# Optimization experiments

Measured on AMD Instinct MI355X. Metric: run time of the kernel, lower is better.

Reference implementation:

```python
import jax, jax.numpy as jnp
import numpy as np

BB_SCALE_TYPE = 'MinMax'  # init kwarg; one of MinMax/Min/Max


def _unproject_all(depth_map, intrinsics):
    # depth_map: [H, W]; returns per-pixel 3D points [H, W, 3]
    H, W = depth_map.shape
    fx, fy, cx, cy = intrinsics[0], intrinsics[1], intrinsics[2], intrinsics[3]
    xs = jnp.arange(W, dtype=depth_map.dtype)[None, :]   # x_d (column)
    ys = jnp.arange(H, dtype=depth_map.dtype)[:, None]   # y_d (row)
    x3 = (xs - cx) * depth_map / fx
    y3 = (ys - cy) * depth_map / fy
    return jnp.stack([x3, y3, depth_map], axis=-1)  # [H, W, 3]


def _scale_to_unit(points, mask):
    # points: [H, W, 3]; mask: [H, W] bool. Masked bbox min/max then norm.
    m = mask[..., None]
    big = jnp.asarray(jnp.finfo(points.dtype).max, points.dtype)
    max_b = jnp.max(jnp.where(m, points, -big), axis=(0, 1))  # [3]
    min_b = jnp.min(jnp.where(m, points, big), axis=(0, 1))   # [3]
    if BB_SCALE_TYPE == 'MinMax':
        return jnp.linalg.norm(max_b - min_b)
    if BB_SCALE_TYPE == 'Min':
        return jnp.linalg.norm(min_b)
    return jnp.linalg.norm(max_b)


def setup_inputs() -> dict:
    key = jax.random.key(0)
    k1, k2, k3 = jax.random.split(key, 3)
    H, W = 2048, 2048
    depth_estimations = jax.random.uniform(k1, (1, 1, H, W), jnp.float32) * 10.0 + 0.1
    sparse_depths = jax.random.uniform(k2, (1, 1, H, W), jnp.float32) * 10.0 + 0.1
    sparse_depth_masks = jax.random.randint(k3, (1, 1, H, W), 0, 2, jnp.int32)
    intrinsics = jnp.array([500.0, 500.0, 1024.0, 1024.0], jnp.float32)  # fx, fy, cx, cy
    return {
        'depth_estimations': depth_estimations,
        'sparse_depths': sparse_depths,
        'sparse_depth_masks': sparse_depth_masks,
        'intrinsics': intrinsics,
    }


def reference(depth_estimations, sparse_depths, sparse_depth_masks, intrinsics):
    mask = sparse_depth_masks[0, 0] != 0  # [H, W]
    pts_sparse = _unproject_all(sparse_depths[0, 0], intrinsics)
    pts_dense = _unproject_all(depth_estimations[0, 0], intrinsics)
    scale_sparse = _scale_to_unit(pts_sparse, mask)
    scale_dense = _scale_to_unit(pts_dense, mask)
    rescaled_depth = (scale_sparse / scale_dense) * depth_estimations
    std = jnp.asarray(1.0, depth_estimations.dtype)
    return (rescaled_depth, std)
```

## Files before the change

### kernel.cpp

```cpp
#include <hip/hip_runtime.h>
#include <float.h>
#include <math.h>

static constexpr int H    = 2048;
static constexpr int Wd   = 2048;
static constexpr int NPIX = H * Wd;
static constexpr int BT   = 256;
static constexpr int N4   = NPIX / 4;

static constexpr int NB1   = 1024;
static constexpr int ITER1 = N4 / (NB1 * BT);

static constexpr int NB2   = 2048;
static constexpr int ITER2 = N4 / (NB2 * BT);


__global__ __launch_bounds__(BT) void reduce_bbox_kernel(
    const float* __restrict__ dense,
    const float* __restrict__ sparse,
    const int*   __restrict__ mask,
    const float* __restrict__ intr,
    float* __restrict__ ws)
{
    const float cx = intr[2], cy = intr[3];
    const float qnan = __uint_as_float(0x7FC00000u);

    float loc[12];
#pragma unroll
    for (int s = 0; s < 12; ++s) loc[s] = ((s % 6) < 3) ? FLT_MAX : -FLT_MAX;

    const float4* d4 = (const float4*)dense;
    const float4* s4 = (const float4*)sparse;
    const int4*   m4 = (const int4*)mask;

    const int tid = blockIdx.x * BT + threadIdx.x;

#pragma unroll
    for (int k = 0; k < ITER1; ++k) {
        const int i = tid + k * (NB1 * BT);
        int4   mv = m4[i];
        float4 dv = d4[i];
        float4 sv = s4[i];
        int base = i << 2;
        float yc = (float)(base >> 11) - cy;
        float xf = (float)(base & 2047);

        const int   mm[4] = { mv.x, mv.y, mv.z, mv.w };
        const float dd[4] = { dv.x, dv.y, dv.z, dv.w };
        const float ss[4] = { sv.x, sv.y, sv.z, sv.w };

#pragma unroll
        for (int j = 0; j < 4; ++j) {
            float sd = (mm[j] != 0) ? ss[j] : qnan;
            float de = (mm[j] != 0) ? dd[j] : qnan;
            float xc = xf + (float)j - cx;
            float spx = xc * sd;
            float spy = yc * sd;
            float dpx = xc * de;
            float dpy = yc * de;
            loc[0] = fminf(loc[0], spx); loc[3]  = fmaxf(loc[3],  spx);
            loc[1] = fminf(loc[1], spy); loc[4]  = fmaxf(loc[4],  spy);
            loc[2] = fminf(loc[2], sd ); loc[5]  = fmaxf(loc[5],  sd );
            loc[6] = fminf(loc[6], dpx); loc[9]  = fmaxf(loc[9],  dpx);
            loc[7] = fminf(loc[7], dpy); loc[10] = fmaxf(loc[10], dpy);
            loc[8] = fminf(loc[8], de ); loc[11] = fmaxf(loc[11], de );
        }
    }

#pragma unroll
    for (int off = 32; off > 0; off >>= 1) {
#pragma unroll
        for (int s = 0; s < 12; ++s) {
            float o = __shfl_xor(loc[s], off, 64);
            loc[s] = ((s % 6) < 3) ? fminf(loc[s], o) : fmaxf(loc[s], o);
        }
    }

    __shared__ float red[4][12];
    int lane = threadIdx.x & 63;
    int wid  = threadIdx.x >> 6;
    if (lane == 0) {
#pragma unroll
        for (int s = 0; s < 12; ++s) red[wid][s] = loc[s];
    }
    __syncthreads();

    if (threadIdx.x < 12) {
        int s = threadIdx.x;
        bool is_min = (s % 6) < 3;
        float v = red[0][s];
#pragma unroll
        for (int w = 1; w < 4; ++w)
            v = is_min ? fminf(v, red[w][s]) : fmaxf(v, red[w][s]);
        ws[s * NB1 + blockIdx.x] = v;
    }
}

__global__ __launch_bounds__(BT) void finalize_scale_kernel(
    const float* __restrict__ dense,
    const float* __restrict__ intr,
    const float* __restrict__ ws,
    float* __restrict__ out)
{
    float loc[12];
#pragma unroll
    for (int s = 0; s < 12; ++s) loc[s] = ((s % 6) < 3) ? FLT_MAX : -FLT_MAX;

    for (int b = threadIdx.x; b < NB1; b += BT) {
#pragma unroll
        for (int s = 0; s < 12; ++s) {
            float p = ws[s * NB1 + b];
            loc[s] = ((s % 6) < 3) ? fminf(loc[s], p) : fmaxf(loc[s], p);
        }
    }

#pragma unroll
    for (int off = 32; off > 0; off >>= 1) {
#pragma unroll
        for (int s = 0; s < 12; ++s) {
            float o = __shfl_xor(loc[s], off, 64);
            loc[s] = ((s % 6) < 3) ? fminf(loc[s], o) : fmaxf(loc[s], o);
        }
    }

    __shared__ float red[4][12];
    __shared__ float ratio_sh;
    int lane = threadIdx.x & 63;
    int wid  = threadIdx.x >> 6;
    if (lane == 0) {
#pragma unroll
        for (int s = 0; s < 12; ++s) red[wid][s] = loc[s];
    }
    __syncthreads();

    if (threadIdx.x == 0) {
        float fin[12];
#pragma unroll
        for (int s = 0; s < 12; ++s) {
            bool is_min = (s % 6) < 3;
            float v = red[0][s];
#pragma unroll
            for (int w = 1; w < 4; ++w)
                v = is_min ? fminf(v, red[w][s]) : fmaxf(v, red[w][s]);
            fin[s] = v;
        }
        const float inv_fx = 1.0f / intr[0], inv_fy = 1.0f / intr[1];
        float sx = (fin[3]  - fin[0]) * inv_fx;
        float sy = (fin[4]  - fin[1]) * inv_fy;
        float sz =  fin[5]  - fin[2];
        float dx = (fin[9]  - fin[6]) * inv_fx;
        float dy = (fin[10] - fin[7]) * inv_fy;
        float dz =  fin[11] - fin[8];
        ratio_sh = sqrtf(sx*sx + sy*sy + sz*sz) / sqrtf(dx*dx + dy*dy + dz*dz);
    }
    __syncthreads();

    const float r = ratio_sh;
    const float4* dv4 = (const float4*)dense;
    float4*       o4  = (float4*)out;
    const int tid = blockIdx.x * BT + threadIdx.x;
#pragma unroll
    for (int k = 0; k < ITER2; ++k) {
        const int i = tid + k * (NB2 * BT);
        float4 v = dv4[i];
        o4[i] = make_float4(v.x * r, v.y * r, v.z * r, v.w * r);
    }
    if (blockIdx.x == 0 && threadIdx.x == 0) out[NPIX] = 1.0f;
}

extern "C" void kernel_launch(void* const* d_in, const int* in_sizes, int n_in,
                              void* d_out, int out_size, void* d_ws, size_t ws_size,
                              hipStream_t stream) {
    const float* dense  = (const float*)d_in[0];
    const float* sparse = (const float*)d_in[1];
    const int*   mask   = (const int*)d_in[2];
    const float* intr   = (const float*)d_in[3];

    float* out  = (float*)d_out;
    float* ws_f = (float*)d_ws;

    reduce_bbox_kernel<<<NB1, BT, 0, stream>>>(dense, sparse, mask, intr, ws_f);
    finalize_scale_kernel<<<NB2, BT, 0, stream>>>(dense, intr, ws_f, out);
}
```

Before: 26.71 us.

## Fuse bbox reduction and rescale into one cooperative kernel keeping dense in registers

Merges the two kernels into a single cooperative launch that uses a grid-wide sync between the per-block bbox reduction and the final ratio computation. Each thread keeps its dense-depth float4 values in registers across the sync, so the rescale pass does not reread the dense map from memory. This saves one kernel launch and a 16 MB reread. In exchange it adds grid-sync cost, requires all 1024 blocks to be co-resident, and raises register pressure (ITER=4 float4s per thread).

```diff
diff --git a/kernel.cpp b/kernel.cpp
--- a/kernel.cpp
+++ b/kernel.cpp
@@ -1,33 +1,28 @@
 #include <hip/hip_runtime.h>
+#include <hip/hip_cooperative_groups.h>
 #include <float.h>
-#include <math.h>
+
+namespace cg = cooperative_groups;
 
 static constexpr int H    = 2048;
 static constexpr int Wd   = 2048;
 static constexpr int NPIX = H * Wd;
 static constexpr int BT   = 256;
 static constexpr int N4   = NPIX / 4;
-
-static constexpr int NB1   = 1024;
-static constexpr int ITER1 = N4 / (NB1 * BT);
-
-static constexpr int NB2   = 2048;
-static constexpr int ITER2 = N4 / (NB2 * BT);
+static constexpr int NB   = 1024;
+static constexpr int ITER = N4 / (NB * BT);
 
 
-__global__ __launch_bounds__(BT) void reduce_bbox_kernel(
+__global__ __launch_bounds__(BT) void fused_depth_scale_kernel(
     const float* __restrict__ dense,
     const float* __restrict__ sparse,
     const int*   __restrict__ mask,
     const float* __restrict__ intr,
-    float* __restrict__ ws)
+    float* __restrict__ ws,
+    float* __restrict__ out)
 {
     const float cx = intr[2], cy = intr[3];
     const float qnan = __uint_as_float(0x7FC00000u);
-
-    float loc[12];
-#pragma unroll
-    for (int s = 0; s < 12; ++s) loc[s] = ((s % 6) < 3) ? FLT_MAX : -FLT_MAX;
 
     const float4* d4 = (const float4*)dense;
     const float4* s4 = (const float4*)sparse;
@@ -35,18 +30,24 @@
 
     const int tid = blockIdx.x * BT + threadIdx.x;
 
+    float loc[12];
 #pragma unroll
-    for (int k = 0; k < ITER1; ++k) {
-        const int i = tid + k * (NB1 * BT);
+    for (int s = 0; s < 12; ++s) loc[s] = ((s % 6) < 3) ? FLT_MAX : -FLT_MAX;
+
+    float4 dv[ITER];
+
+#pragma unroll
+    for (int k = 0; k < ITER; ++k) {
+        const int i = tid + k * (NB * BT);
         int4   mv = m4[i];
-        float4 dv = d4[i];
+        dv[k]     = d4[i];
         float4 sv = s4[i];
         int base = i << 2;
         float yc = (float)(base >> 11) - cy;
         float xf = (float)(base & 2047);
 
         const int   mm[4] = { mv.x, mv.y, mv.z, mv.w };
-        const float dd[4] = { dv.x, dv.y, dv.z, dv.w };
+        const float dd[4] = { dv[k].x, dv[k].y, dv[k].z, dv[k].w };
         const float ss[4] = { sv.x, sv.y, sv.z, sv.w };
 
 #pragma unroll
@@ -77,8 +78,9 @@
     }
 
     __shared__ float red[4][12];
-    int lane = threadIdx.x & 63;
-    int wid  = threadIdx.x >> 6;
+    __shared__ float ratio_sh;
+    const int lane = threadIdx.x & 63;
+    const int wid  = threadIdx.x >> 6;
     if (lane == 0) {
 #pragma unroll
         for (int s = 0; s < 12; ++s) red[wid][s] = loc[s];
@@ -92,25 +94,20 @@
 #pragma unroll
         for (int w = 1; w < 4; ++w)
             v = is_min ? fminf(v, red[w][s]) : fmaxf(v, red[w][s]);
-        ws[s * NB1 + blockIdx.x] = v;
+        ws[s * NB + blockIdx.x] = v;
     }
-}
 
-__global__ __launch_bounds__(BT) void finalize_scale_kernel(
-    const float* __restrict__ dense,
-    const float* __restrict__ intr,
-    const float* __restrict__ ws,
-    float* __restrict__ out)
-{
-    float loc[12];
+    cg::this_grid().sync();
+
+    float loc2[12];
 #pragma unroll
-    for (int s = 0; s < 12; ++s) loc[s] = ((s % 6) < 3) ? FLT_MAX : -FLT_MAX;
+    for (int s = 0; s < 12; ++s) loc2[s] = ((s % 6) < 3) ? FLT_MAX : -FLT_MAX;
 
-    for (int b = threadIdx.x; b < NB1; b += BT) {
+    for (int b = threadIdx.x; b < NB; b += BT) {
 #pragma unroll
         for (int s = 0; s < 12; ++s) {
-            float p = ws[s * NB1 + b];
-            loc[s] = ((s % 6) < 3) ? fminf(loc[s], p) : fmaxf(loc[s], p);
+            float p = ws[s * NB + b];
+            loc2[s] = ((s % 6) < 3) ? fminf(loc2[s], p) : fmaxf(loc2[s], p);
         }
     }
 
@@ -118,18 +115,14 @@
     for (int off = 32; off > 0; off >>= 1) {
 #pragma unroll
         for (int s = 0; s < 12; ++s) {
-            float o = __shfl_xor(loc[s], off, 64);
-            loc[s] = ((s % 6) < 3) ? fminf(loc[s], o) : fmaxf(loc[s], o);
+            float o = __shfl_xor(loc2[s], off, 64);
+            loc2[s] = ((s % 6) < 3) ? fminf(loc2[s], o) : fmaxf(loc2[s], o);
         }
     }
 
-    __shared__ float red[4][12];
-    __shared__ float ratio_sh;
-    int lane = threadIdx.x & 63;
-    int wid  = threadIdx.x >> 6;
     if (lane == 0) {
 #pragma unroll
-        for (int s = 0; s < 12; ++s) red[wid][s] = loc[s];
+        for (int s = 0; s < 12; ++s) red[wid][s] = loc2[s];
     }
     __syncthreads();
 
@@ -156,13 +149,11 @@
     __syncthreads();
 
     const float r = ratio_sh;
-    const float4* dv4 = (const float4*)dense;
-    float4*       o4  = (float4*)out;
-    const int tid = blockIdx.x * BT + threadIdx.x;
+    float4* o4 = (float4*)out;
 #pragma unroll
-    for (int k = 0; k < ITER2; ++k) {
-        const int i = tid + k * (NB2 * BT);
-        float4 v = dv4[i];
+    for (int k = 0; k < ITER; ++k) {
+        const int i = tid + k * (NB * BT);
+        float4 v = dv[k];
         o4[i] = make_float4(v.x * r, v.y * r, v.z * r, v.w * r);
     }
     if (blockIdx.x == 0 && threadIdx.x == 0) out[NPIX] = 1.0f;
@@ -179,6 +170,8 @@
     float* out  = (float*)d_out;
     float* ws_f = (float*)d_ws;
 
-    reduce_bbox_kernel<<<NB1, BT, 0, stream>>>(dense, sparse, mask, intr, ws_f);
-    finalize_scale_kernel<<<NB2, BT, 0, stream>>>(dense, intr, ws_f, out);
+    void* args[] = { (void*)&dense, (void*)&sparse, (void*)&mask,
+                     (void*)&intr, (void*)&ws_f, (void*)&out };
+    hipLaunchCooperativeKernel((const void*)fused_depth_scale_kernel,
+                               dim3(NB), dim3(BT), args, 0, stream);
 }
```

After: 106.5 us. +299.0%, slower.
